# Optimization experiments

Hardware: AMD Instinct MI355X
Metric: run time of the kernel (lower is better)

Reference implementation:

```python
import jax, jax.numpy as jnp
import numpy as np

BN_EPS = 1e-5


def _bn(x, g, b):
    # torch BatchNorm1d training-mode forward: biased batch stats over active sites
    m = x.mean(axis=0)
    v = x.var(axis=0)
    return (x - m) * jax.lax.rsqrt(v + BN_EPS) * g + b


def _subm_conv(h, nbr_idx, Wk):
    # submanifold kxk conv via rulebook: for each kernel offset, gather active
    # neighbors (idx >= 0), GEMM with that offset's weight, accumulate.
    out = jnp.zeros((h.shape[0], Wk.shape[2]), dtype=h.dtype)
    for k in range(Wk.shape[0]):  # fixed small loop over 9 kernel offsets
        idx = nbr_idx[:, k]
        mask = (idx >= 0).astype(h.dtype)[:, None]
        g = h[jnp.clip(idx, 0)] * mask  # [N, Cmid]
        out = out + g @ Wk[k]
    return out


def setup_inputs() -> dict:
    B, H, W = 4, 512, 512
    N = 260000
    Cin, Cout, K = 64, 256, 3
    Cmid = Cout // 4
    rng = np.random.default_rng(0)
    # random active sites (unique), like an occupied BEV grid
    lin = rng.choice(B * H * W, size=N, replace=False)
    b = lin // (H * W)
    rem = lin % (H * W)
    y = rem // W
    x = rem % W
    grid = -np.ones(B * H * W, dtype=np.int32)
    grid[lin] = np.arange(N, dtype=np.int32)
    nbr = np.full((N, K * K), -1, dtype=np.int32)
    k = 0
    for dy in (-1, 0, 1):
        for dx in (-1, 0, 1):
            yy = y + dy
            xx = x + dx
            valid = (yy >= 0) & (yy < H) & (xx >= 0) & (xx < W)
            li = (b * H + np.clip(yy, 0, H - 1)) * W + np.clip(xx, 0, W - 1)
            nbr[:, k] = np.where(valid, grid[li], -1)
            k += 1
    key = jax.random.key(0)
    ks = jax.random.split(key, 6)
    s_in = 1.0 / np.sqrt(Cin)
    s_mid = 1.0 / np.sqrt(Cmid * K * K)
    s_m1 = 1.0 / np.sqrt(Cmid)
    return {
        "features": jax.random.normal(ks[0], (N, Cin), jnp.float32),
        "nbr_idx": jnp.asarray(nbr),
        "W1": jax.random.normal(ks[1], (Cin, Cmid), jnp.float32) * s_in,
        "g1": jnp.ones((Cmid,), jnp.float32),
        "b1": jnp.zeros((Cmid,), jnp.float32),
        "Wk": jax.random.normal(ks[2], (K * K, Cmid, Cmid), jnp.float32) * s_mid,
        "g2": jnp.ones((Cmid,), jnp.float32),
        "b2": jnp.zeros((Cmid,), jnp.float32),
        "W3": jax.random.normal(ks[3], (Cmid, Cout), jnp.float32) * s_m1,
        "g3": jnp.ones((Cout,), jnp.float32),
        "b3": jnp.zeros((Cout,), jnp.float32),
        "Ws": jax.random.normal(ks[4], (Cin, Cout), jnp.float32) * s_in,
        "gs": jnp.ones((Cout,), jnp.float32),
        "bs": jnp.zeros((Cout,), jnp.float32),
    }


def reference(features, nbr_idx, W1, g1, b1, Wk, g2, b2, W3, g3, b3, Ws, gs, bs):
    # bottleneck branch: 1x1 -> BN -> ReLU -> kxk subm -> BN -> ReLU -> 1x1 -> BN
    h = jax.nn.relu(_bn(features @ W1, g1, b1))
    h = jax.nn.relu(_bn(_subm_conv(h, nbr_idx, Wk), g2, b2))
    y = _bn(h @ W3, g3, b3)
    # shortcut branch: 1x1 -> BN
    s = _bn(features @ Ws, gs, bs)
    # sparse_add: identical active-site sets (submanifold) -> elementwise add
    return jax.nn.relu(y + s)
```

## Files before the change

kernel.cpp:

```cpp
#include <hip/hip_runtime.h>

typedef __attribute__((ext_vector_type(8))) short  s16x8;
typedef __attribute__((ext_vector_type(8))) unsigned short u16x8;
typedef __attribute__((ext_vector_type(4))) float  f32x4;

constexpr float BN_EPS = 1e-5f;
#define DEV_INLINE __device__ __forceinline__

DEV_INLINE ushort f2bf(float f) {
  unsigned int u = __float_as_uint(f);
  return (ushort)((u + 0x7FFFu + ((u >> 16) & 1u)) >> 16);
}
DEV_INLINE float bf2f(ushort b) { return __uint_as_float(((unsigned int)b) << 16); }

DEV_INLINE unsigned int cvtpk(float a, float b) {
  unsigned int r;
  asm volatile("v_cvt_pk_bf16_f32 %0, %1, %2" : "=v"(r) : "v"(a), "v"(b));
  return r;
}

DEV_INLINE f32x4 mfma16(s16x8 a, s16x8 b, f32x4 c) {
  return __builtin_amdgcn_mfma_f32_16x16x32_bf16(a, b, c, 0, 0, 0);
}

DEV_INLINE void decode_frag(int r, int& k, int& c16) {
  const int ks = r >> 9;
  const int l = (r >> 3) & 63;
  const int j = r & 7;
  k = ks * 32 + ((l >> 4) << 3) + j;
  c16 = l & 15;
}

__global__ void kPackW(const float* __restrict__ W1, const float* __restrict__ Ws,
                       const float* __restrict__ Wk, const float* __restrict__ W3,
                       ushort* __restrict__ WP1S, ushort* __restrict__ WPk,
                       ushort* __restrict__ WP3, float* __restrict__ statz) {
  int e = blockIdx.x * 256 + threadIdx.x;
  if (e < 1280) statz[e] = 0.f;
  if (e < 20480) {
    int ct = e >> 10, r = e & 1023, k, c16;
    decode_frag(r, k, c16);
    float w = (ct < 4) ? W1[k * 64 + ct * 16 + c16] : Ws[k * 256 + (ct - 4) * 16 + c16];
    WP1S[e] = f2bf(w);
  } else if (e < 57344) {
    int e2 = e - 20480;
    int tap = e2 >> 12, r2 = e2 & 4095;
    int ct = r2 >> 10, k, c16;
    decode_frag(r2 & 1023, k, c16);
    WPk[e2] = f2bf(Wk[tap * 4096 + k * 64 + ct * 16 + c16]);
  } else {
    int e3 = e - 57344;
    int ct = e3 >> 10, k, c16;
    decode_frag(e3 & 1023, k, c16);
    WP3[e3] = f2bf(W3[k * 256 + ct * 16 + c16]);
  }
}

DEV_INLINE void bnFin(const float* sum, const float* sq, const float* g,
                      const float* b, float invN, int j, float* a_lds, float* c_lds) {
  float m = sum[j] * invN;
  float v = fmaxf(sq[j] * invN - m * m, 0.f);
  float al = g[j] * rsqrtf(v + BN_EPS);
  a_lds[j] = al;
  c_lds[j] = fmaf(-m, al, b[j]);
}

__global__ __launch_bounds__(256) void kStatsXW(const float* __restrict__ X,
                                                const ushort* __restrict__ WP,
                                                ushort* __restrict__ Xb,
                                                float* __restrict__ gsum,
                                                float* __restrict__ gsq,
                                                int N, int ntiles) {
  __shared__ ushort At[64 * 64];
  const int tid = threadIdx.x;
  const int l = tid & 63, w = tid >> 6;
  const int kb = (l >> 4) << 4;
  const int r = tid >> 2, q = tid & 3;
  const int sww = (r & 7) << 4;
  const u16x8* wp = (const u16x8*)WP;
  s16x8 wgt[5][2];
#pragma unroll
  for (int i = 0; i < 5; ++i)
#pragma unroll
    for (int j = 0; j < 2; ++j) wgt[i][j] = (s16x8)wp[((w * 5 + i) * 2 + j) * 64 + l];
  float sA[5] = {0.f, 0.f, 0.f, 0.f, 0.f}, qA[5] = {0.f, 0.f, 0.f, 0.f, 0.f};
  for (int t = blockIdx.x; t < ntiles; t += gridDim.x) {
    const int row0 = t * 64;
    const int grow = row0 + r;
    u16x8 lo = {0, 0, 0, 0, 0, 0, 0, 0}, hi = {0, 0, 0, 0, 0, 0, 0, 0};
    if (grow < N) {
      const float4* xp = reinterpret_cast<const float4*>(&X[(size_t)grow * 64 + q * 16]);
      float4 x0 = xp[0], x1 = xp[1], x2 = xp[2], x3 = xp[3];
      union { u16x8 v; unsigned int d[4]; } ul, uh;
      ul.d[0] = cvtpk(x0.x, x0.y); ul.d[1] = cvtpk(x0.z, x0.w);
      ul.d[2] = cvtpk(x1.x, x1.y); ul.d[3] = cvtpk(x1.z, x1.w);
      uh.d[0] = cvtpk(x2.x, x2.y); uh.d[1] = cvtpk(x2.z, x2.w);
      uh.d[2] = cvtpk(x3.x, x3.y); uh.d[3] = cvtpk(x3.z, x3.w);
      lo = ul.v; hi = uh.v;
      *(u16x8*)&Xb[(size_t)grow * 64 + q * 16] = lo;
      *(u16x8*)&Xb[(size_t)grow * 64 + q * 16 + 8] = hi;
    }
    __syncthreads();
    char* wb = (char*)At + r * 128;
    *(u16x8*)(wb + ((q * 32) ^ sww)) = lo;
    *(u16x8*)(wb + ((q * 32 + 16) ^ sww)) = hi;
    __syncthreads();
#pragma unroll
    for (int rb = 0; rb < 4; ++rb) {
      const int rowa = rb * 16 + (l & 15);
      const char* ab = (const char*)At + rowa * 128;
      const int swa = (rowa & 7) << 4;
      const s16x8 a0 = *(const s16x8*)(ab + (kb ^ swa));
      const s16x8 a1 = *(const s16x8*)(ab + ((64 + kb) ^ swa));
#pragma unroll
      for (int i = 0; i < 5; ++i) {
        f32x4 acc = {0.f, 0.f, 0.f, 0.f};
        acc = mfma16(a0, wgt[i][0], acc);
        acc = mfma16(a1, wgt[i][1], acc);
        sA[i] += acc[0] + acc[1] + acc[2] + acc[3];
        qA[i] += acc[0] * acc[0] + acc[1] * acc[1] + acc[2] * acc[2] + acc[3] * acc[3];
      }
    }
  }
#pragma unroll
  for (int i = 0; i < 5; ++i) {
    float sp = sA[i], qp = qA[i];
    sp += __shfl_xor(sp, 16); sp += __shfl_xor(sp, 32);
    qp += __shfl_xor(qp, 16); qp += __shfl_xor(qp, 32);
    if (l < 16) {
      atomicAdd(&gsum[(w * 5 + i) * 16 + l], sp);
      atomicAdd(&gsq[(w * 5 + i) * 16 + l], qp);
    }
  }
}

__global__ __launch_bounds__(256) void kGemm1(const ushort* __restrict__ Xb,
                                              const ushort* __restrict__ WP,
                                              const float* __restrict__ sum1,
                                              const float* __restrict__ sq1,
                                              const float* __restrict__ g1,
                                              const float* __restrict__ b1,
                                              float invN, ushort* __restrict__ H1,
                                              int N, int ntiles) {
  __shared__ ushort At[64 * 64];
  __shared__ float a1s[64], c1s[64];
  const int tid = threadIdx.x;
  if (tid < 64) bnFin(sum1, sq1, g1, b1, invN, tid, a1s, c1s);
  const int l = tid & 63, w = tid >> 6;
  const int kb = (l >> 4) << 4;
  const int r = tid >> 2, q = tid & 3;
  const int sww = (r & 7) << 4;
  const u16x8* wp = (const u16x8*)WP;
  const s16x8 wg0 = (s16x8)wp[(w * 2 + 0) * 64 + l];
  const s16x8 wg1 = (s16x8)wp[(w * 2 + 1) * 64 + l];
  const int col = w * 16 + (l & 15);
  for (int t = blockIdx.x; t < ntiles; t += gridDim.x) {
    const int row0 = t * 64;
    const int grow = row0 + r;
    u16x8 lo = {0, 0, 0, 0, 0, 0, 0, 0}, hi = {0, 0, 0, 0, 0, 0, 0, 0};
    if (grow < N) {
      const u16x8* hp = (const u16x8*)&Xb[(size_t)grow * 64 + q * 16];
      lo = hp[0];
      hi = hp[1];
    }
    __syncthreads();
    char* wb = (char*)At + r * 128;
    *(u16x8*)(wb + ((q * 32) ^ sww)) = lo;
    *(u16x8*)(wb + ((q * 32 + 16) ^ sww)) = hi;
    __syncthreads();
    const float aj = a1s[col], cj = c1s[col];
#pragma unroll
    for (int rb = 0; rb < 4; ++rb) {
      const int rowa = rb * 16 + (l & 15);
      const char* ab = (const char*)At + rowa * 128;
      const int swa = (rowa & 7) << 4;
      const s16x8 a0 = *(const s16x8*)(ab + (kb ^ swa));
      const s16x8 a1 = *(const s16x8*)(ab + ((64 + kb) ^ swa));
      f32x4 acc = {0.f, 0.f, 0.f, 0.f};
      acc = mfma16(a0, wg0, acc);
      acc = mfma16(a1, wg1, acc);
#pragma unroll
      for (int reg = 0; reg < 4; ++reg) {
        const int gr = row0 + rb * 16 + ((l >> 4) << 2) + reg;
        if (gr < N)
          H1[(size_t)gr * 64 + col] =
              (ushort)cvtpk(fmaxf(fmaf(acc[reg], aj, cj), 0.f), 0.f);
      }
    }
  }
}

__global__ __launch_bounds__(256) void kConv(const ushort* __restrict__ H1,
                                             const int* __restrict__ nbr,
                                             const ushort* __restrict__ WPk,
                                             ushort* __restrict__ Y2b,
                                             float* __restrict__ gsum,
                                             float* __restrict__ gsq,
                                             int N, int ntiles, int tpb) {
  __shared__ float lsum[64], lsq[64];
  const int tid = threadIdx.x;
  if (tid < 64) { lsum[tid] = 0.f; lsq[tid] = 0.f; }
  __syncthreads();
  const int l = tid & 63, w = tid >> 6;
  const int lr = l & 15;
  const int ks = l >> 4;
  const u16x8* wp = (const u16x8*)WPk;
  float sAcc[4] = {0.f, 0.f, 0.f, 0.f}, qAcc[4] = {0.f, 0.f, 0.f, 0.f};
  const int t0 = blockIdx.x * tpb;
  const int t1 = (t0 + tpb < ntiles) ? (t0 + tpb) : ntiles;
  const s16x8 zf = {0, 0, 0, 0, 0, 0, 0, 0};
  for (int t = t0; t < t1; ++t) {
    const int row = t * 64 + w * 16 + lr;
    const bool valid = row < N;
    int srcs[9];
#pragma unroll
    for (int k = 0; k < 9; ++k)
      srcs[k] = valid ? nbr[(size_t)row * 9 + k] : -1;
    s16x8 A0[9], A1[9];
#pragma unroll
    for (int k = 0; k < 9; ++k) {
      const int sc = (srcs[k] < 0) ? 0 : srcs[k];
      const char* p = (const char*)H1 + (size_t)sc * 128 + ks * 16;
      A0[k] = *(const s16x8*)p;
      A1[k] = *(const s16x8*)(p + 64);
    }
#pragma unroll
    for (int k = 0; k < 9; ++k) {
      if (srcs[k] < 0) { A0[k] = zf; A1[k] = zf; }
    }
    f32x4 acc[4];
#pragma unroll
    for (int ct = 0; ct < 4; ++ct) acc[ct] = {0.f, 0.f, 0.f, 0.f};
    __builtin_amdgcn_s_setprio(1);
#pragma unroll
    for (int k = 0; k < 9; ++k) {
#pragma unroll
      for (int ct = 0; ct < 4; ++ct) {
        s16x8 b0 = (s16x8)wp[(size_t)((k * 4 + ct) * 2 + 0) * 64 + l];
        s16x8 b1 = (s16x8)wp[(size_t)((k * 4 + ct) * 2 + 1) * 64 + l];
        acc[ct] = mfma16(A0[k], b0, acc[ct]);
        acc[ct] = mfma16(A1[k], b1, acc[ct]);
      }
    }
    __builtin_amdgcn_s_setprio(0);
#pragma unroll
    for (int ct = 0; ct < 4; ++ct) {
      const f32x4 v = acc[ct];
      const int col = ct * 16 + (l & 15);
#pragma unroll
      for (int reg = 0; reg < 4; ++reg) {
        const int gr = t * 64 + w * 16 + (ks << 2) + reg;
        if (gr < N) Y2b[(size_t)gr * 64 + col] = (ushort)cvtpk(v[reg], v[reg]);
      }
      sAcc[ct] += v[0] + v[1] + v[2] + v[3];
      qAcc[ct] += v[0] * v[0] + v[1] * v[1] + v[2] * v[2] + v[3] * v[3];
    }
  }
#pragma unroll
  for (int ct = 0; ct < 4; ++ct) {
    float sp = sAcc[ct], qp = qAcc[ct];
    sp += __shfl_xor(sp, 16); sp += __shfl_xor(sp, 32);
    qp += __shfl_xor(qp, 16); qp += __shfl_xor(qp, 32);
    if (l < 16) {
      atomicAdd(&lsum[ct * 16 + l], sp);
      atomicAdd(&lsq[ct * 16 + l], qp);
    }
  }
  __syncthreads();
  if (tid < 64) {
    atomicAdd(&gsum[tid], lsum[tid]);
    atomicAdd(&gsq[tid], lsq[tid]);
  }
}

__global__ __launch_bounds__(256) void kH2S3(const ushort* __restrict__ Y2b,
                                             const float* __restrict__ sum2,
                                             const float* __restrict__ sq2,
                                             const float* __restrict__ g2,
                                             const float* __restrict__ b2,
                                             float invN,
                                             const ushort* __restrict__ WP3,
                                             float* __restrict__ gsum,
                                             float* __restrict__ gsq,
                                             int N, int ntiles) {
  __shared__ ushort At[64 * 64];
  __shared__ float a2s[64], c2s[64];
  const int tid = threadIdx.x;
  if (tid < 64) bnFin(sum2, sq2, g2, b2, invN, tid, a2s, c2s);
  const int l = tid & 63, w = tid >> 6;
  const int kb = (l >> 4) << 4;
  const int r = tid >> 2, q = tid & 3;
  const int sww = (r & 7) << 4;
  const u16x8* wp = (const u16x8*)WP3;
  s16x8 wgt[4][2];
#pragma unroll
  for (int i = 0; i < 4; ++i)
#pragma unroll
    for (int j = 0; j < 2; ++j) wgt[i][j] = (s16x8)wp[((w * 4 + i) * 2 + j) * 64 + l];
  float sA[4] = {0.f, 0.f, 0.f, 0.f}, qA[4] = {0.f, 0.f, 0.f, 0.f};
  __syncthreads();
  for (int t = blockIdx.x; t < ntiles; t += gridDim.x) {
    const int row0 = t * 64;
    const int grow = row0 + r;
    u16x8 lo = {0, 0, 0, 0, 0, 0, 0, 0}, hi = {0, 0, 0, 0, 0, 0, 0, 0};
    if (grow < N) {
      const u16x8* yp = (const u16x8*)&Y2b[(size_t)grow * 64 + q * 16];
      u16x8 ylo = yp[0], yhi = yp[1];
      const int cb = q * 16;
      float f[8], g[8];
#pragma unroll
      for (int i = 0; i < 8; ++i) {
        f[i] = fmaxf(fmaf(bf2f(ylo[i]), a2s[cb + i], c2s[cb + i]), 0.f);
        g[i] = fmaxf(fmaf(bf2f(yhi[i]), a2s[cb + 8 + i], c2s[cb + 8 + i]), 0.f);
      }
      union { u16x8 v; unsigned int d[4]; } ul, uh;
#pragma unroll
      for (int i = 0; i < 4; ++i) {
        ul.d[i] = cvtpk(f[2 * i], f[2 * i + 1]);
        uh.d[i] = cvtpk(g[2 * i], g[2 * i + 1]);
      }
      lo = ul.v; hi = uh.v;
    }
    __syncthreads();
    char* wb = (char*)At + r * 128;
    *(u16x8*)(wb + ((q * 32) ^ sww)) = lo;
    *(u16x8*)(wb + ((q * 32 + 16) ^ sww)) = hi;
    __syncthreads();
#pragma unroll
    for (int rb = 0; rb < 4; ++rb) {
      const int rowa = rb * 16 + (l & 15);
      const char* ab = (const char*)At + rowa * 128;
      const int swa = (rowa & 7) << 4;
      const s16x8 a0 = *(const s16x8*)(ab + (kb ^ swa));
      const s16x8 a1 = *(const s16x8*)(ab + ((64 + kb) ^ swa));
#pragma unroll
      for (int i = 0; i < 4; ++i) {
        f32x4 acc = {0.f, 0.f, 0.f, 0.f};
        acc = mfma16(a0, wgt[i][0], acc);
        acc = mfma16(a1, wgt[i][1], acc);
        sA[i] += acc[0] + acc[1] + acc[2] + acc[3];
        qA[i] += acc[0] * acc[0] + acc[1] * acc[1] + acc[2] * acc[2] + acc[3] * acc[3];
      }
    }
  }
#pragma unroll
  for (int i = 0; i < 4; ++i) {
    float sp = sA[i], qp = qA[i];
    sp += __shfl_xor(sp, 16); sp += __shfl_xor(sp, 32);
    qp += __shfl_xor(qp, 16); qp += __shfl_xor(qp, 32);
    if (l < 16) {
      atomicAdd(&gsum[(w * 4 + i) * 16 + l], sp);
      atomicAdd(&gsq[(w * 4 + i) * 16 + l], qp);
    }
  }
}

__global__ __launch_bounds__(256, 2) void kFinal(
    const ushort* __restrict__ Y2b, const ushort* __restrict__ Xb,
    const ushort* __restrict__ WP3, const ushort* __restrict__ WP1S,
    const float* __restrict__ sum2, const float* __restrict__ sq2,
    const float* __restrict__ g2, const float* __restrict__ b2,
    const float* __restrict__ sum3, const float* __restrict__ sq3,
    const float* __restrict__ g3, const float* __restrict__ b3,
    const float* __restrict__ sumS, const float* __restrict__ sqS,
    const float* __restrict__ gs, const float* __restrict__ bs,
    float invN, float* __restrict__ OUT, int N, int ntiles) {
  __shared__ ushort Ah[64 * 64];
  __shared__ ushort Ax[64 * 64];
  __shared__ float a2s[64], c2s[64];
  __shared__ float a3s[256], c3s[256], aSs[256], cSs[256];
  const int tid = threadIdx.x;
  if (tid < 64) bnFin(sum2, sq2, g2, b2, invN, tid, a2s, c2s);
  bnFin(sum3, sq3, g3, b3, invN, tid, a3s, c3s);
  bnFin(sumS, sqS, gs, bs, invN, tid, aSs, cSs);
  const int l = tid & 63, w = tid >> 6;
  const int kb = (l >> 4) << 4;
  const int r = tid >> 2, q = tid & 3;
  const int sww = (r & 7) << 4;
  const u16x8* wp3 = (const u16x8*)WP3;
  const u16x8* wps = (const u16x8*)WP1S + 8 * 64;
  s16x8 w3[4][2], wsv[4][2];
#pragma unroll
  for (int i = 0; i < 4; ++i)
#pragma unroll
    for (int j = 0; j < 2; ++j) {
      w3[i][j]  = (s16x8)wp3[((w * 4 + i) * 2 + j) * 64 + l];
      wsv[i][j] = (s16x8)wps[((w * 4 + i) * 2 + j) * 64 + l];
    }
  __syncthreads();
  float a3r[4], aSr[4], ccr[4];
#pragma unroll
  for (int i = 0; i < 4; ++i) {
    const int col = (w * 4 + i) * 16 + (l & 15);
    a3r[i] = a3s[col];
    aSr[i] = aSs[col];
    ccr[i] = c3s[col] + cSs[col];
  }
  for (int t = blockIdx.x; t < ntiles; t += gridDim.x) {
    const int row0 = t * 64;
    const int grow = row0 + r;
    u16x8 xlo = {0, 0, 0, 0, 0, 0, 0, 0}, xhi = {0, 0, 0, 0, 0, 0, 0, 0};
    u16x8 hlo = {0, 0, 0, 0, 0, 0, 0, 0}, hhi = {0, 0, 0, 0, 0, 0, 0, 0};
    if (grow < N) {
      const u16x8* hp = (const u16x8*)&Xb[(size_t)grow * 64 + q * 16];
      xlo = hp[0];
      xhi = hp[1];
      const u16x8* yp = (const u16x8*)&Y2b[(size_t)grow * 64 + q * 16];
      u16x8 ylo = yp[0], yhi = yp[1];
      const int cb = q * 16;
      float f[8], g[8];
#pragma unroll
      for (int i = 0; i < 8; ++i) {
        f[i] = fmaxf(fmaf(bf2f(ylo[i]), a2s[cb + i], c2s[cb + i]), 0.f);
        g[i] = fmaxf(fmaf(bf2f(yhi[i]), a2s[cb + 8 + i], c2s[cb + 8 + i]), 0.f);
      }
      union { u16x8 v; unsigned int d[4]; } ul, uh;
#pragma unroll
      for (int i = 0; i < 4; ++i) {
        ul.d[i] = cvtpk(f[2 * i], f[2 * i + 1]);
        uh.d[i] = cvtpk(g[2 * i], g[2 * i + 1]);
      }
      hlo = ul.v; hhi = uh.v;
    }
    __syncthreads();
    {
      char* bh = (char*)Ah + r * 128;
      char* bx = (char*)Ax + r * 128;
      *(u16x8*)(bh + ((q * 32) ^ sww)) = hlo;
      *(u16x8*)(bh + ((q * 32 + 16) ^ sww)) = hhi;
      *(u16x8*)(bx + ((q * 32) ^ sww)) = xlo;
      *(u16x8*)(bx + ((q * 32 + 16) ^ sww)) = xhi;
    }
    __syncthreads();
#pragma unroll
    for (int rb = 0; rb < 4; ++rb) {
      const int rowa = rb * 16 + (l & 15);
      const int swa = (rowa & 7) << 4;
      const char* hb = (const char*)Ah + rowa * 128;
      const char* xb2 = (const char*)Ax + rowa * 128;
      const s16x8 ah0 = *(const s16x8*)(hb + (kb ^ swa));
      const s16x8 ah1 = *(const s16x8*)(hb + ((64 + kb) ^ swa));
      const s16x8 ax0 = *(const s16x8*)(xb2 + (kb ^ swa));
      const s16x8 ax1 = *(const s16x8*)(xb2 + ((64 + kb) ^ swa));
#pragma unroll
      for (int i = 0; i < 4; ++i) {
        const int col = (w * 4 + i) * 16 + (l & 15);
        f32x4 acc3 = {0.f, 0.f, 0.f, 0.f};
        acc3 = mfma16(ah0, w3[i][0], acc3);
        acc3 = mfma16(ah1, w3[i][1], acc3);
        f32x4 accS = {0.f, 0.f, 0.f, 0.f};
        accS = mfma16(ax0, wsv[i][0], accS);
        accS = mfma16(ax1, wsv[i][1], accS);
#pragma unroll
        for (int reg = 0; reg < 4; ++reg) {
          const int gr = row0 + rb * 16 + ((l >> 4) << 2) + reg;
          if (gr < N) {
            const float ov =
                fmaxf(fmaf(acc3[reg], a3r[i], fmaf(accS[reg], aSr[i], ccr[i])), 0.f);
            __builtin_nontemporal_store(ov, &OUT[(size_t)gr * 256 + col]);
          }
        }
      }
    }
  }
}

extern "C" void kernel_launch(void* const* d_in, const int* in_sizes, int n_in,
                              void* d_out, int out_size, void* d_ws, size_t ws_size,
                              hipStream_t stream) {
  const float* X  = (const float*)d_in[0];
  const int*   nbr = (const int*)d_in[1];
  const float* W1 = (const float*)d_in[2];
  const float* g1 = (const float*)d_in[3];
  const float* b1 = (const float*)d_in[4];
  const float* Wk = (const float*)d_in[5];
  const float* g2 = (const float*)d_in[6];
  const float* b2 = (const float*)d_in[7];
  const float* W3 = (const float*)d_in[8];
  const float* g3 = (const float*)d_in[9];
  const float* b3 = (const float*)d_in[10];
  const float* Ws = (const float*)d_in[11];
  const float* gs = (const float*)d_in[12];
  const float* bs = (const float*)d_in[13];
  float* out = (float*)d_out;
  float* ws  = (float*)d_ws;

  const int N = in_sizes[0] / 64;
  const float invN = 1.f / (float)N;
  const int ntiles = (N + 63) / 64;

  float* sum1S = ws + 0;
  float* sq1S  = ws + 320;
  float* sum2  = ws + 640;
  float* sq2   = ws + 704;
  float* sum3  = ws + 768;
  float* sq3   = ws + 1024;
  ushort* WP1S = (ushort*)(ws + 1280);
  ushort* WPkP = (ushort*)(ws + 11520);
  ushort* WP3P = (ushort*)(ws + 29952);
  ushort* Xb   = (ushort*)(ws + 38144);
  ushort* Y2b  = (ushort*)(ws + 38144 + (size_t)N * 32);
  ushort* H1b  = (ushort*)(ws + 38144 + (size_t)N * 64);

  const int convGrid = 1024;
  const int tpb = (ntiles + convGrid - 1) / convGrid;

  kPackW<<<288, 256, 0, stream>>>(W1, Ws, Wk, W3, WP1S, WPkP, WP3P, ws);
  kStatsXW<<<508, 256, 0, stream>>>(X, WP1S, Xb, sum1S, sq1S, N, ntiles);
  kGemm1<<<508, 256, 0, stream>>>(Xb, WP1S, sum1S, sq1S, g1, b1, invN, H1b, N, ntiles);
  kConv<<<convGrid, 256, 0, stream>>>(H1b, nbr, WPkP, Y2b, sum2, sq2, N, ntiles, tpb);
  kH2S3<<<508, 256, 0, stream>>>(Y2b, sum2, sq2, g2, b2, invN, WP3P, sum3, sq3, N, ntiles);
  kFinal<<<512, 256, 0, stream>>>(Y2b, Xb, WP3P, WP1S, sum2, sq2, g2, b2,
                                  sum3, sq3, g3, b3, sum1S + 64, sq1S + 64,
                                  gs, bs, invN, out, N, ntiles);
}
```

Baseline: 226.6 us.

## Load MFMA A-fragments directly from global memory, dropping LDS staging and barriers

Four kernels (stats, gemm1, H2 stats, final) no longer stage 64-row tiles through swizzled LDS with two __syncthreads per tile. Each lane now loads its MFMA A-fragment straight from global memory, or L2, and converts it in registers. BN finalize coefficients are computed per lane into registers instead of being broadcast through shared memory. This removes the barriers and LDS traffic, but every wave now re-reads the same rows, up to 4x redundant global/L2 loads and, in the stats kernel, redundant fp32-to-bf16 conversion. The min-blocks hint on kFinal is also dropped.

After: 256.8 us. 13.3% more time.

```diff
diff --git a/kernel.cpp b/kernel.cpp
--- a/kernel.cpp
+++ b/kernel.cpp
@@ -29,6 +29,15 @@
   const int j = r & 7;
   k = ks * 32 + ((l >> 4) << 3) + j;
   c16 = l & 15;
+}
+
+DEV_INLINE void bnFinReg(const float* __restrict__ sum, const float* __restrict__ sq,
+                         const float* __restrict__ g, const float* __restrict__ b,
+                         float invN, int ch, float& a, float& c) {
+  float m = sum[ch] * invN;
+  float v = fmaxf(sq[ch] * invN - m * m, 0.f);
+  a = g[ch] * rsqrtf(v + BN_EPS);
+  c = fmaf(-m, a, b[ch]);
 }
 
 __global__ void kPackW(const float* __restrict__ W1, const float* __restrict__ Ws,
@@ -56,13 +65,18 @@
   }
 }
 
-DEV_INLINE void bnFin(const float* sum, const float* sq, const float* g,
-                      const float* b, float invN, int j, float* a_lds, float* c_lds) {
-  float m = sum[j] * invN;
-  float v = fmaxf(sq[j] * invN - m * m, 0.f);
-  float al = g[j] * rsqrtf(v + BN_EPS);
-  a_lds[j] = al;
-  c_lds[j] = fmaf(-m, al, b[j]);
+DEV_INLINE void loadFragF32(const float* __restrict__ X, int row, int ks,
+                            s16x8& a0, s16x8& a1) {
+  const float4* p0 = reinterpret_cast<const float4*>(X + (size_t)row * 64 + ks * 8);
+  const float4* p1 = reinterpret_cast<const float4*>(X + (size_t)row * 64 + 32 + ks * 8);
+  float4 x0 = p0[0], x1 = p0[1], y0 = p1[0], y1 = p1[1];
+  union { s16x8 v; unsigned int d[4]; } u0, u1;
+  u0.d[0] = cvtpk(x0.x, x0.y); u0.d[1] = cvtpk(x0.z, x0.w);
+  u0.d[2] = cvtpk(x1.x, x1.y); u0.d[3] = cvtpk(x1.z, x1.w);
+  u1.d[0] = cvtpk(y0.x, y0.y); u1.d[1] = cvtpk(y0.z, y0.w);
+  u1.d[2] = cvtpk(y1.x, y1.y); u1.d[3] = cvtpk(y1.z, y1.w);
+  a0 = u0.v;
+  a1 = u1.v;
 }
 
 __global__ __launch_bounds__(256) void kStatsXW(const float* __restrict__ X,
@@ -71,47 +85,30 @@
                                                 float* __restrict__ gsum,
                                                 float* __restrict__ gsq,
                                                 int N, int ntiles) {
-  __shared__ ushort At[64 * 64];
   const int tid = threadIdx.x;
   const int l = tid & 63, w = tid >> 6;
-  const int kb = (l >> 4) << 4;
-  const int r = tid >> 2, q = tid & 3;
-  const int sww = (r & 7) << 4;
+  const int j = l & 15, ks = l >> 4;
   const u16x8* wp = (const u16x8*)WP;
   s16x8 wgt[5][2];
 #pragma unroll
   for (int i = 0; i < 5; ++i)
 #pragma unroll
-    for (int j = 0; j < 2; ++j) wgt[i][j] = (s16x8)wp[((w * 5 + i) * 2 + j) * 64 + l];
+    for (int jj = 0; jj < 2; ++jj) wgt[i][jj] = (s16x8)wp[((w * 5 + i) * 2 + jj) * 64 + l];
   float sA[5] = {0.f, 0.f, 0.f, 0.f, 0.f}, qA[5] = {0.f, 0.f, 0.f, 0.f, 0.f};
+  const s16x8 zf = {0, 0, 0, 0, 0, 0, 0, 0};
   for (int t = blockIdx.x; t < ntiles; t += gridDim.x) {
-    const int row0 = t * 64;
-    const int grow = row0 + r;
-    u16x8 lo = {0, 0, 0, 0, 0, 0, 0, 0}, hi = {0, 0, 0, 0, 0, 0, 0, 0};
-    if (grow < N) {
-      const float4* xp = reinterpret_cast<const float4*>(&X[(size_t)grow * 64 + q * 16]);
-      float4 x0 = xp[0], x1 = xp[1], x2 = xp[2], x3 = xp[3];
-      union { u16x8 v; unsigned int d[4]; } ul, uh;
-      ul.d[0] = cvtpk(x0.x, x0.y); ul.d[1] = cvtpk(x0.z, x0.w);
-      ul.d[2] = cvtpk(x1.x, x1.y); ul.d[3] = cvtpk(x1.z, x1.w);
-      uh.d[0] = cvtpk(x2.x, x2.y); uh.d[1] = cvtpk(x2.z, x2.w);
-      uh.d[2] = cvtpk(x3.x, x3.y); uh.d[3] = cvtpk(x3.z, x3.w);
-      lo = ul.v; hi = uh.v;
-      *(u16x8*)&Xb[(size_t)grow * 64 + q * 16] = lo;
-      *(u16x8*)&Xb[(size_t)grow * 64 + q * 16 + 8] = hi;
-    }
-    __syncthreads();
-    char* wb = (char*)At + r * 128;
-    *(u16x8*)(wb + ((q * 32) ^ sww)) = lo;
-    *(u16x8*)(wb + ((q * 32 + 16) ^ sww)) = hi;
-    __syncthreads();
 #pragma unroll
     for (int rb = 0; rb < 4; ++rb) {
-      const int rowa = rb * 16 + (l & 15);
-      const char* ab = (const char*)At + rowa * 128;
-      const int swa = (rowa & 7) << 4;
-      const s16x8 a0 = *(const s16x8*)(ab + (kb ^ swa));
-      const s16x8 a1 = *(const s16x8*)(ab + ((64 + kb) ^ swa));
+      const int row = t * 64 + rb * 16 + j;
+      s16x8 a0 = zf, a1 = zf;
+      if (row < N) {
+        loadFragF32(X, row, ks, a0, a1);
+        if (rb == w) {
+          char* xp = (char*)Xb + (size_t)row * 128 + ks * 16;
+          *(s16x8*)xp = a0;
+          *(s16x8*)(xp + 64) = a1;
+        }
+      }
 #pragma unroll
       for (int i = 0; i < 5; ++i) {
         f32x4 acc = {0.f, 0.f, 0.f, 0.f};
@@ -142,46 +139,32 @@
                                               const float* __restrict__ b1,
                                               float invN, ushort* __restrict__ H1,
                                               int N, int ntiles) {
-  __shared__ ushort At[64 * 64];
-  __shared__ float a1s[64], c1s[64];
   const int tid = threadIdx.x;
-  if (tid < 64) bnFin(sum1, sq1, g1, b1, invN, tid, a1s, c1s);
   const int l = tid & 63, w = tid >> 6;
-  const int kb = (l >> 4) << 4;
-  const int r = tid >> 2, q = tid & 3;
-  const int sww = (r & 7) << 4;
+  const int j = l & 15, ks = l >> 4;
   const u16x8* wp = (const u16x8*)WP;
   const s16x8 wg0 = (s16x8)wp[(w * 2 + 0) * 64 + l];
   const s16x8 wg1 = (s16x8)wp[(w * 2 + 1) * 64 + l];
-  const int col = w * 16 + (l & 15);
+  const int col = w * 16 + j;
+  float aj, cj;
+  bnFinReg(sum1, sq1, g1, b1, invN, col, aj, cj);
+  const s16x8 zf = {0, 0, 0, 0, 0, 0, 0, 0};
   for (int t = blockIdx.x; t < ntiles; t += gridDim.x) {
-    const int row0 = t * 64;
-    const int grow = row0 + r;
-    u16x8 lo = {0, 0, 0, 0, 0, 0, 0, 0}, hi = {0, 0, 0, 0, 0, 0, 0, 0};
-    if (grow < N) {
-      const u16x8* hp = (const u16x8*)&Xb[(size_t)grow * 64 + q * 16];
-      lo = hp[0];
-      hi = hp[1];
-    }
-    __syncthreads();
-    char* wb = (char*)At + r * 128;
-    *(u16x8*)(wb + ((q * 32) ^ sww)) = lo;
-    *(u16x8*)(wb + ((q * 32 + 16) ^ sww)) = hi;
-    __syncthreads();
-    const float aj = a1s[col], cj = c1s[col];
 #pragma unroll
     for (int rb = 0; rb < 4; ++rb) {
-      const int rowa = rb * 16 + (l & 15);
-      const char* ab = (const char*)At + rowa * 128;
-      const int swa = (rowa & 7) << 4;
-      const s16x8 a0 = *(const s16x8*)(ab + (kb ^ swa));
-      const s16x8 a1 = *(const s16x8*)(ab + ((64 + kb) ^ swa));
+      const int row = t * 64 + rb * 16 + j;
+      s16x8 a0 = zf, a1 = zf;
+      if (row < N) {
+        const char* xp = (const char*)Xb + (size_t)row * 128 + ks * 16;
+        a0 = *(const s16x8*)xp;
+        a1 = *(const s16x8*)(xp + 64);
+      }
       f32x4 acc = {0.f, 0.f, 0.f, 0.f};
       acc = mfma16(a0, wg0, acc);
       acc = mfma16(a1, wg1, acc);
 #pragma unroll
       for (int reg = 0; reg < 4; ++reg) {
-        const int gr = row0 + rb * 16 + ((l >> 4) << 2) + reg;
+        const int gr = t * 64 + rb * 16 + ks * 4 + reg;
         if (gr < N)
           H1[(size_t)gr * 64 + col] =
               (ushort)cvtpk(fmaxf(fmaf(acc[reg], aj, cj), 0.f), 0.f);
@@ -246,10 +229,10 @@
 #pragma unroll
     for (int ct = 0; ct < 4; ++ct) {
       const f32x4 v = acc[ct];
-      const int col = ct * 16 + (l & 15);
+      const int col = ct * 16 + lr;
 #pragma unroll
       for (int reg = 0; reg < 4; ++reg) {
-        const int gr = t * 64 + w * 16 + (ks << 2) + reg;
+        const int gr = t * 64 + w * 16 + ks * 4 + reg;
         if (gr < N) Y2b[(size_t)gr * 64 + col] = (ushort)cvtpk(v[reg], v[reg]);
       }
       sAcc[ct] += v[0] + v[1] + v[2] + v[3];
@@ -271,6 +254,28 @@
     atomicAdd(&gsum[tid], lsum[tid]);
     atomicAdd(&gsq[tid], lsq[tid]);
   }
+}
+
+DEV_INLINE void loadFragH2(const ushort* __restrict__ Y2b, int row, int ks,
+                           const float* a2v, const float* c2v,
+                           s16x8& h0, s16x8& h1) {
+  const char* yp = (const char*)Y2b + (size_t)row * 128 + ks * 16;
+  u16x8 y0 = *(const u16x8*)yp;
+  u16x8 y1 = *(const u16x8*)(yp + 64);
+  float f[8], g[8];
+#pragma unroll
+  for (int i = 0; i < 8; ++i) {
+    f[i] = fmaxf(fmaf(bf2f(y0[i]), a2v[i], c2v[i]), 0.f);
+    g[i] = fmaxf(fmaf(bf2f(y1[i]), a2v[8 + i], c2v[8 + i]), 0.f);
+  }
+  union { s16x8 v; unsigned int d[4]; } u0, u1;
+#pragma unroll
+  for (int i = 0; i < 4; ++i) {
+    u0.d[i] = cvtpk(f[2 * i], f[2 * i + 1]);
+    u1.d[i] = cvtpk(g[2 * i], g[2 * i + 1]);
+  }
+  h0 = u0.v;
+  h1 = u1.v;
 }
 
 __global__ __launch_bounds__(256) void kH2S3(const ushort* __restrict__ Y2b,
@@ -283,61 +288,34 @@
                                              float* __restrict__ gsum,
                                              float* __restrict__ gsq,
                                              int N, int ntiles) {
-  __shared__ ushort At[64 * 64];
-  __shared__ float a2s[64], c2s[64];
   const int tid = threadIdx.x;
-  if (tid < 64) bnFin(sum2, sq2, g2, b2, invN, tid, a2s, c2s);
   const int l = tid & 63, w = tid >> 6;
-  const int kb = (l >> 4) << 4;
-  const int r = tid >> 2, q = tid & 3;
-  const int sww = (r & 7) << 4;
+  const int j = l & 15, ks = l >> 4;
   const u16x8* wp = (const u16x8*)WP3;
   s16x8 wgt[4][2];
 #pragma unroll
   for (int i = 0; i < 4; ++i)
 #pragma unroll
-    for (int j = 0; j < 2; ++j) wgt[i][j] = (s16x8)wp[((w * 4 + i) * 2 + j) * 64 + l];
+    for (int jj = 0; jj < 2; ++jj) wgt[i][jj] = (s16x8)wp[((w * 4 + i) * 2 + jj) * 64 + l];
+  float a2v[16], c2v[16];
+#pragma unroll
+  for (int i = 0; i < 8; ++i) {
+    bnFinReg(sum2, sq2, g2, b2, invN, ks * 8 + i, a2v[i], c2v[i]);
+    bnFinReg(sum2, sq2, g2, b2, invN, 32 + ks * 8 + i, a2v[8 + i], c2v[8 + i]);
+  }
   float sA[4] = {0.f, 0.f, 0.f, 0.f}, qA[4] = {0.f, 0.f, 0.f, 0.f};
-  __syncthreads();
+  const s16x8 zf = {0, 0, 0, 0, 0, 0, 0, 0};
   for (int t = blockIdx.x; t < ntiles; t += gridDim.x) {
-    const int row0 = t * 64;
-    const int grow = row0 + r;
-    u16x8 lo = {0, 0, 0, 0, 0, 0, 0, 0}, hi = {0, 0, 0, 0, 0, 0, 0, 0};
-    if (grow < N) {
-      const u16x8* yp = (const u16x8*)&Y2b[(size_t)grow * 64 + q * 16];
-      u16x8 ylo = yp[0], yhi = yp[1];
-      const int cb = q * 16;
-      float f[8], g[8];
-#pragma unroll
-      for (int i = 0; i < 8; ++i) {
-        f[i] = fmaxf(fmaf(bf2f(ylo[i]), a2s[cb + i], c2s[cb + i]), 0.f);
-        g[i] = fmaxf(fmaf(bf2f(yhi[i]), a2s[cb + 8 + i], c2s[cb + 8 + i]), 0.f);
-      }
-      union { u16x8 v; unsigned int d[4]; } ul, uh;
-#pragma unroll
-      for (int i = 0; i < 4; ++i) {
-        ul.d[i] = cvtpk(f[2 * i], f[2 * i + 1]);
-        uh.d[i] = cvtpk(g[2 * i], g[2 * i + 1]);
-      }
-      lo = ul.v; hi = uh.v;
-    }
-    __syncthreads();
-    char* wb = (char*)At + r * 128;
-    *(u16x8*)(wb + ((q * 32) ^ sww)) = lo;
-    *(u16x8*)(wb + ((q * 32 + 16) ^ sww)) = hi;
-    __syncthreads();
 #pragma unroll
     for (int rb = 0; rb < 4; ++rb) {
-      const int rowa = rb * 16 + (l & 15);
-      const char* ab = (const char*)At + rowa * 128;
-      const int swa = (rowa & 7) << 4;
-      const s16x8 a0 = *(const s16x8*)(ab + (kb ^ swa));
-      const s16x8 a1 = *(const s16x8*)(ab + ((64 + kb) ^ swa));
+      const int row = t * 64 + rb * 16 + j;
+      s16x8 h0 = zf, h1 = zf;
+      if (row < N) loadFragH2(Y2b, row, ks, a2v, c2v, h0, h1);
 #pragma unroll
       for (int i = 0; i < 4; ++i) {
         f32x4 acc = {0.f, 0.f, 0.f, 0.f};
-        acc = mfma16(a0, wgt[i][0], acc);
-        acc = mfma16(a1, wgt[i][1], acc);
+        acc = mfma16(h0, wgt[i][0], acc);
+        acc = mfma16(h1, wgt[i][1], acc);
         sA[i] += acc[0] + acc[1] + acc[2] + acc[3];
         qA[i] += acc[0] * acc[0] + acc[1] * acc[1] + acc[2] * acc[2] + acc[3] * acc[3];
       }
@@ -355,7 +333,7 @@
   }
 }
 
-__global__ __launch_bounds__(256, 2) void kFinal(
+__global__ __launch_bounds__(256) void kFinal(
     const ushort* __restrict__ Y2b, const ushort* __restrict__ Xb,
     const ushort* __restrict__ WP3, const ushort* __restrict__ WP1S,
     const float* __restrict__ sum2, const float* __restrict__ sq2,
@@ -365,86 +343,51 @@
     const float* __restrict__ sumS, const float* __restrict__ sqS,
     const float* __restrict__ gs, const float* __restrict__ bs,
     float invN, float* __restrict__ OUT, int N, int ntiles) {
-  __shared__ ushort Ah[64 * 64];
-  __shared__ ushort Ax[64 * 64];
-  __shared__ float a2s[64], c2s[64];
-  __shared__ float a3s[256], c3s[256], aSs[256], cSs[256];
   const int tid = threadIdx.x;
-  if (tid < 64) bnFin(sum2, sq2, g2, b2, invN, tid, a2s, c2s);
-  bnFin(sum3, sq3, g3, b3, invN, tid, a3s, c3s);
-  bnFin(sumS, sqS, gs, bs, invN, tid, aSs, cSs);
   const int l = tid & 63, w = tid >> 6;
-  const int kb = (l >> 4) << 4;
-  const int r = tid >> 2, q = tid & 3;
-  const int sww = (r & 7) << 4;
+  const int j = l & 15, ks = l >> 4;
   const u16x8* wp3 = (const u16x8*)WP3;
   const u16x8* wps = (const u16x8*)WP1S + 8 * 64;
   s16x8 w3[4][2], wsv[4][2];
 #pragma unroll
   for (int i = 0; i < 4; ++i)
 #pragma unroll
-    for (int j = 0; j < 2; ++j) {
-      w3[i][j]  = (s16x8)wp3[((w * 4 + i) * 2 + j) * 64 + l];
-      wsv[i][j] = (s16x8)wps[((w * 4 + i) * 2 + j) * 64 + l];
-    }
-  __syncthreads();
+    for (int jj = 0; jj < 2; ++jj) {
+      w3[i][jj]  = (s16x8)wp3[((w * 4 + i) * 2 + jj) * 64 + l];
+      wsv[i][jj] = (s16x8)wps[((w * 4 + i) * 2 + jj) * 64 + l];
+    }
+  float a2v[16], c2v[16];
+#pragma unroll
+  for (int i = 0; i < 8; ++i) {
+    bnFinReg(sum2, sq2, g2, b2, invN, ks * 8 + i, a2v[i], c2v[i]);
+    bnFinReg(sum2, sq2, g2, b2, invN, 32 + ks * 8 + i, a2v[8 + i], c2v[8 + i]);
+  }
   float a3r[4], aSr[4], ccr[4];
 #pragma unroll
   for (int i = 0; i < 4; ++i) {
-    const int col = (w * 4 + i) * 16 + (l & 15);
-    a3r[i] = a3s[col];
-    aSr[i] = aSs[col];
-    ccr[i] = c3s[col] + cSs[col];
-  }
+    const int col = (w * 4 + i) * 16 + j;
+    float a3, c3, aS, cS;
+    bnFinReg(sum3, sq3, g3, b3, invN, col, a3, c3);
+    bnFinReg(sumS, sqS, gs, bs, invN, col, aS, cS);
+    a3r[i] = a3;
+    aSr[i] = aS;
+    ccr[i] = c3 + cS;
+  }
+  const s16x8 zf = {0, 0, 0, 0, 0, 0, 0, 0};
   for (int t = blockIdx.x; t < ntiles; t += gridDim.x) {
-    const int row0 = t * 64;
-    const int grow = row0 + r;
-    u16x8 xlo = {0, 0, 0, 0, 0, 0, 0, 0}, xhi = {0, 0, 0, 0, 0, 0, 0, 0};
-    u16x8 hlo = {0, 0, 0, 0, 0, 0, 0, 0}, hhi = {0, 0, 0, 0, 0, 0, 0, 0};
-    if (grow < N) {
-      const u16x8* hp = (const u16x8*)&Xb[(size_t)grow * 64 + q * 16];
-      xlo = hp[0];
-      xhi = hp[1];
-      const u16x8* yp = (const u16x8*)&Y2b[(size_t)grow * 64 + q * 16];
-      u16x8 ylo = yp[0], yhi = yp[1];
-      const int cb = q * 16;
-      float f[8], g[8];
-#pragma unroll
-      for (int i = 0; i < 8; ++i) {
-        f[i] = fmaxf(fmaf(bf2f(ylo[i]), a2s[cb + i], c2s[cb + i]), 0.f);
-        g[i] = fmaxf(fmaf(bf2f(yhi[i]), a2s[cb + 8 + i], c2s[cb + 8 + i]), 0.f);
-      }
-      union { u16x8 v; unsigned int d[4]; } ul, uh;
+#pragma unroll
+    for (int rb = 0; rb < 4; ++rb) {
+      const int row = t * 64 + rb * 16 + j;
+      s16x8 ah0 = zf, ah1 = zf, ax0 = zf, ax1 = zf;
+      if (row < N) {
+        loadFragH2(Y2b, row, ks, a2v, c2v, ah0, ah1);
+        const char* xp = (const char*)Xb + (size_t)row * 128 + ks * 16;
+        ax0 = *(const s16x8*)xp;
+        ax1 = *(const s16x8*)(xp + 64);
+      }
 #pragma unroll
       for (int i = 0; i < 4; ++i) {
-        ul.d[i] = cvtpk(f[2 * i], f[2 * i + 1]);
-        uh.d[i] = cvtpk(g[2 * i], g[2 * i + 1]);
-      }
-      hlo = ul.v; hhi = uh.v;
-    }
-    __syncthreads();
-    {
-      char* bh = (char*)Ah + r * 128;
-      char* bx = (char*)Ax + r * 128;
-      *(u16x8*)(bh + ((q * 32) ^ sww)) = hlo;
-      *(u16x8*)(bh + ((q * 32 + 16) ^ sww)) = hhi;
-      *(u16x8*)(bx + ((q * 32) ^ sww)) = xlo;
-      *(u16x8*)(bx + ((q * 32 + 16) ^ sww)) = xhi;
-    }
-    __syncthreads();
-#pragma unroll
-    for (int rb = 0; rb < 4; ++rb) {
-      const int rowa = rb * 16 + (l & 15);
-      const int swa = (rowa & 7) << 4;
-      const char* hb = (const char*)Ah + rowa * 128;
-      const char* xb2 = (const char*)Ax + rowa * 128;
-      const s16x8 ah0 = *(const s16x8*)(hb + (kb ^ swa));
-      const s16x8 ah1 = *(const s16x8*)(hb + ((64 + kb) ^ swa));
-      const s16x8 ax0 = *(const s16x8*)(xb2 + (kb ^ swa));
-      const s16x8 ax1 = *(const s16x8*)(xb2 + ((64 + kb) ^ swa));
-#pragma unroll
-      for (int i = 0; i < 4; ++i) {
-        const int col = (w * 4 + i) * 16 + (l & 15);
+        const int col = (w * 4 + i) * 16 + j;
         f32x4 acc3 = {0.f, 0.f, 0.f, 0.f};
         acc3 = mfma16(ah0, w3[i][0], acc3);
         acc3 = mfma16(ah1, w3[i][1], acc3);
@@ -453,7 +396,7 @@
         accS = mfma16(ax1, wsv[i][1], accS);
 #pragma unroll
         for (int reg = 0; reg < 4; ++reg) {
-          const int gr = row0 + rb * 16 + ((l >> 4) << 2) + reg;
+          const int gr = t * 64 + rb * 16 + ks * 4 + reg;
           if (gr < N) {
             const float ov =
                 fmaxf(fmaf(acc3[reg], a3r[i], fmaf(accS[reg], aSr[i], ccr[i])), 0.f);
```
